# Kernel tuning notes

Measured on AMD Instinct MI355X. Metric: run time of the kernel, lower is better.

## Reference

```python
import jax, jax.numpy as jnp
import numpy as np

NQ = 10000   # num_q
N = 512      # n (seq len)
D = 512      # d (model dim)
H = 8        # attention heads
LW = 64      # local window
B = 16       # batch


def _mha(q, k, v, wi, bi, wo, bo, nh, mask=None):
    # torch nn.MultiheadAttention math (eval mode, dropout off), batch-first inputs
    Bq, S, d = q.shape
    hd = d // nh
    wq, wk, wv = jnp.split(wi, 3, axis=0)
    bq, bk, bv = jnp.split(bi, 3)

    def proj(x, w, b):
        y = x @ w.T + b
        return y.reshape(x.shape[0], x.shape[1], nh, hd).transpose(0, 2, 1, 3)  # [B,h,S,hd]

    Q = proj(q, wq, bq)
    K = proj(k, wk, bk)
    V = proj(v, wv, bv)
    s = jnp.einsum('bhqe,bhke->bhqk', Q, K) / jnp.sqrt(jnp.asarray(hd, q.dtype))
    if mask is not None:
        s = jnp.where(mask[None, None], -jnp.inf, s)
    w = jax.nn.softmax(s, axis=-1)
    o = jnp.einsum('bhqk,bhke->bhqe', w, V).transpose(0, 2, 1, 3).reshape(Bq, S, d)
    return o @ wo.T + bo, w.mean(axis=1)  # avg over heads like torch default


def _ln(x, g, b):
    m = x.mean(-1, keepdims=True)
    v = ((x - m) ** 2).mean(-1, keepdims=True)
    return (x - m) / jnp.sqrt(v + 1e-5) * g + b


def setup_inputs() -> dict:
    key = jax.random.key(0)
    ks = iter(jax.random.split(key, 40))
    f = lambda *sh: jax.random.normal(next(ks), sh, jnp.float32) * 0.02
    inp = {
        'q': jax.random.randint(next(ks), (B, N), 0, NQ, jnp.int32),
        'r': jax.random.randint(next(ks), (B, N), 0, 2, jnp.int32),
        'qry': jax.random.randint(next(ks), (B, N), 0, NQ, jnp.int32),
        'M_emb': f(2 * NQ, D),
        'E_emb': f(NQ, D),
        'P': f(N, D),
    }
    for nm in ['base', 'local', 'glob', 'cross']:
        inp[nm + '_in_w'] = f(3 * D, D)
        inp[nm + '_in_b'] = jnp.zeros((3 * D,), jnp.float32)
        inp[nm + '_out_w'] = f(D, D)
        inp[nm + '_out_b'] = jnp.zeros((D,), jnp.float32)
    inp['ln1_g'] = jnp.ones((D,), jnp.float32)
    inp['ln1_b'] = jnp.zeros((D,), jnp.float32)
    inp['w1'] = f(D, D)
    inp['b1'] = jnp.zeros((D,), jnp.float32)
    inp['w2'] = f(D, D)
    inp['b2'] = jnp.zeros((D,), jnp.float32)
    inp['ln2_g'] = jnp.ones((D,), jnp.float32)
    inp['ln2_b'] = jnp.zeros((D,), jnp.float32)
    inp['pred_w'] = f(1, D)
    inp['pred_b'] = jnp.zeros((1,), jnp.float32)
    return inp


def reference(q, r, qry, M_emb, E_emb, P,
              base_in_w, base_in_b, base_out_w, base_out_b,
              local_in_w, local_in_b, local_out_w, local_out_b,
              glob_in_w, glob_in_b, glob_out_w, glob_out_b,
              cross_in_w, cross_in_b, cross_out_w, cross_out_b,
              ln1_g, ln1_b, w1, b1, w2, b2, ln2_g, ln2_b, pred_w, pred_b):
    x = q + NQ * r
    M = M_emb[x] + P[None]          # [B,N,D], positional added as in torch code
    E = E_emb[qry]                  # [B,N,D]
    cm = jnp.triu(jnp.ones((N, N), bool), 1)

    S_base, attn_w = _mha(E, M, M, base_in_w, base_in_b, base_out_w, base_out_b, H, cm)
    S_base = _ln(S_base + M + E, ln1_g, ln1_b)

    lm = jnp.triu(jnp.ones((LW, LW), bool), 1)
    s_loc_in = S_base[:, -LW:, :]
    S_loc, _ = _mha(s_loc_in, s_loc_in, s_loc_in, local_in_w, local_in_b, local_out_w, local_out_b, H, lm)
    S_local = jnp.concatenate([jnp.zeros((S_base.shape[0], N - LW, D), S_base.dtype), S_loc], axis=1)

    S_global, _ = _mha(S_base, S_base, S_base, glob_in_w, glob_in_b, glob_out_w, glob_out_b, H, cm)
    S_cross, _ = _mha(S_base, S_local, S_local, cross_in_w, cross_in_b, cross_out_w, cross_out_b, H, None)

    S = S_base + S_local + S_global + S_cross
    F = jax.nn.relu(S @ w1.T + b1) @ w2.T + b2
    F = _ln(F + S, ln2_g, ln2_b)
    p = jax.nn.sigmoid(F @ pred_w.T + pred_b)[..., 0]   # [B,N]
    return p, attn_w
```

## Files before the change

kernel.cpp:

```cpp
#include <hip/hip_runtime.h>
#include <hip/hip_bf16.h>

#define D_MODEL 512
#define NHEAD 8
#define NSEQ 512
#define BATCH 16
#define LWIN 64
#define S2C 0.18033688f
#define L2E 1.44269504f

typedef short s16x8 __attribute__((ext_vector_type(8)));
typedef float f32x4 __attribute__((ext_vector_type(4)));

__device__ inline unsigned short f2bf(float f) {
    unsigned int u = __float_as_uint(f);
    u = (u + 0x7fffu + ((u >> 16) & 1u)) >> 16;
    return (unsigned short)u;
}
__device__ inline int sw4(int r) { return (r + (r >> 2)) & 3; }

#define GLD16(g, l) __builtin_amdgcn_global_load_lds( \
    (const __attribute__((address_space(1))) void*)(g), \
    (__attribute__((address_space(3))) void*)(l), 16, 0, 0)

struct WP { const float* p[10]; };
__global__ __launch_bounds__(256) void wconv_kernel(WP wp, unsigned short* __restrict__ Wb)
{
    const long e = ((long)blockIdx.x * 256 + threadIdx.x) * 4;
    const float* src; long loc;
    if (e < 3145728) { int rg = (int)(e / 786432); src = wp.p[rg]; loc = e - (long)rg * 786432; }
    else { long j = e - 3145728; int rg = (int)(j >> 18); src = wp.p[4 + rg]; loc = j - ((long)rg << 18); }
    float4 v = *(const float4*)(src + loc);
    ushort4 o; o.x = f2bf(v.x); o.y = f2bf(v.y); o.z = f2bf(v.z); o.w = f2bf(v.w);
    *(ushort4*)(Wb + e) = o;
}

__global__ __launch_bounds__(128) void embed_kernel(
    const int* __restrict__ q, const int* __restrict__ r, const int* __restrict__ qry,
    const float* __restrict__ M_emb, const float* __restrict__ E_emb,
    const float* __restrict__ P, float* __restrict__ Mf, float* __restrict__ Ef,
    unsigned short* __restrict__ Mb, unsigned short* __restrict__ Eb)
{
    const int t = blockIdx.x;
    const int n = t & (NSEQ - 1);
    const int x = q[t] + 10000 * r[t];
    const int e = qry[t];
    const int i = threadIdx.x;
    float4 a = ((const float4*)(M_emb + (long)x * D_MODEL))[i];
    float4 p4 = ((const float4*)(P + (long)n * D_MODEL))[i];
    float4 ev = ((const float4*)(E_emb + (long)e * D_MODEL))[i];
    float4 mv = make_float4(a.x + p4.x, a.y + p4.y, a.z + p4.z, a.w + p4.w);
    ((float4*)(Mf + (long)t * D_MODEL))[i] = mv;
    ((float4*)(Ef + (long)t * D_MODEL))[i] = ev;
    ushort4 mb; mb.x = f2bf(mv.x); mb.y = f2bf(mv.y); mb.z = f2bf(mv.z); mb.w = f2bf(mv.w);
    ushort4 eb; eb.x = f2bf(ev.x); eb.y = f2bf(ev.y); eb.z = f2bf(ev.z); eb.w = f2bf(ev.w);
    *(ushort4*)(Mb + (long)t * D_MODEL + i * 4) = mb;
    *(ushort4*)(Eb + (long)t * D_MODEL + i * 4) = eb;
}

__global__ __launch_bounds__(256) void zfill_kernel(unsigned short* __restrict__ p)
{
    const long i = ((long)blockIdx.x * 256 + threadIdx.x) * 8;
    *(uint4*)(p + i) = make_uint4(0u, 0u, 0u, 0u);
}

__global__ __launch_bounds__(256) void gemm_bf16(
    const unsigned short* __restrict__ A, const unsigned short* __restrict__ A2, int nsplit,
    const unsigned short* __restrict__ W, const float* __restrict__ bias,
    unsigned short* __restrict__ Cb, int ldcb, int crem,
    float* __restrict__ Cf, int ldcf,
    const float* __restrict__ r1, const float* __restrict__ r2, const float* __restrict__ tl,
    int relu, int arem)
{
    __shared__ __align__(16) unsigned short Sh[8704];
    unsigned short* As = Sh;
    unsigned short* Ws = Sh + 4096;
    float* Shf = (float*)Sh;

    const int tid = threadIdx.x, lane = tid & 63, wid = tid >> 6;
    const int m0 = blockIdx.y * 128, n0 = blockIdx.x * 128;
    const int mbase = (wid >> 1) * 64, nbase = (wid & 1) * 64;
    const int fr = lane & 15;
    const int lq = lane >> 4;
    const unsigned short* Asel = (n0 >= nsplit) ? A2 : A;

    const int rlane = lane >> 2, clane = lane & 3;
    const int lrA0 = wid * 16 + rlane, lrA1 = 64 + wid * 16 + rlane;
    int rgA0 = m0 + lrA0, rgA1 = m0 + lrA1;
    if (arem) {
        rgA0 = ((rgA0 >> 6) << 9) + (NSEQ - LWIN) + (rgA0 & 63);
        rgA1 = ((rgA1 >> 6) << 9) + (NSEQ - LWIN) + (rgA1 & 63);
    }
    const unsigned short* pA0 = Asel + (long)rgA0 * 512 + ((clane ^ sw4(lrA0)) << 3);
    const unsigned short* pA1 = Asel + (long)rgA1 * 512 + ((clane ^ sw4(lrA1)) << 3);
    const unsigned short* pW0 = W + (long)(n0 + lrA0) * 512 + ((clane ^ sw4(lrA0)) << 3);
    const unsigned short* pW1 = W + (long)(n0 + lrA1) * 512 + ((clane ^ sw4(lrA1)) << 3);
    unsigned short* lA0 = As + (wid * 16) * 32;
    unsigned short* lA1 = As + (64 + wid * 16) * 32;
    unsigned short* lW0 = Ws + (wid * 16) * 32;
    unsigned short* lW1 = Ws + (64 + wid * 16) * 32;

    f32x4 acc[4][4];
    #pragma unroll
    for (int i = 0; i < 4; ++i)
        #pragma unroll
        for (int j = 0; j < 4; ++j) acc[i][j] = (f32x4){0.f, 0.f, 0.f, 0.f};

    for (int k0 = 0; k0 < 512; k0 += 32) {
        __syncthreads();
        GLD16(pA0 + k0, lA0);
        GLD16(pA1 + k0, lA1);
        GLD16(pW0 + k0, lW0);
        GLD16(pW1 + k0, lW1);
        __syncthreads();

        s16x8 af[4], wf[4];
        #pragma unroll
        for (int t = 0; t < 4; ++t) {
            const int ra = mbase + t * 16 + fr;
            const int rw = nbase + t * 16 + fr;
            af[t] = *(const s16x8*)&As[ra * 32 + ((lq ^ sw4(ra)) << 3)];
            wf[t] = *(const s16x8*)&Ws[rw * 32 + ((lq ^ sw4(rw)) << 3)];
        }
        #pragma unroll
        for (int i = 0; i < 4; ++i)
            #pragma unroll
            for (int j = 0; j < 4; ++j)
                acc[i][j] = __builtin_amdgcn_mfma_f32_16x16x32_bf16(af[i], wf[j], acc[i][j], 0, 0, 0);
    }

    const int q4 = (lane >> 4) * 4;
    for (int qtr = 0; qtr < 4; ++qtr) {
        __syncthreads();
        if ((wid >> 1) == (qtr >> 1)) {
            const int ibase = (qtr & 1) * 2;
            #pragma unroll
            for (int j = 0; j < 4; ++j) {
                const int lcol = nbase + j * 16 + fr;
                const float bv = bias[n0 + lcol];
                #pragma unroll
                for (int i2 = 0; i2 < 2; ++i2) {
                    const int i = ibase + i2;
                    #pragma unroll
                    for (int rg = 0; rg < 4; ++rg) {
                        float v = acc[i][j][rg] + bv;
                        if (relu) v = fmaxf(v, 0.f);
                        Shf[((i * 16 + q4 + rg) & 31) * 132 + lcol] = v;
                    }
                }
            }
        }
        __syncthreads();
        #pragma unroll
        for (int it = 0; it < 4; ++it) {
            const int flat = it * 256 + tid;
            const int rowq = flat >> 5, k4 = flat & 31;
            const int grow = m0 + qtr * 32 + rowq;
            const int gcol = n0 + k4 * 4;
            float4 f = *(const float4*)&Shf[rowq * 132 + k4 * 4];
            if (r1) {
                float4 a = *(const float4*)(r1 + (long)grow * 512 + gcol);
                float4 b = *(const float4*)(r2 + (long)grow * 512 + gcol);
                f.x += a.x + b.x; f.y += a.y + b.y; f.z += a.z + b.z; f.w += a.w + b.w;
                const int n = grow & 511;
                if (n >= NSEQ - LWIN) {
                    float4 c = *(const float4*)(tl + ((long)(grow >> 9) * 64 + (n - (NSEQ - LWIN))) * 512 + gcol);
                    f.x += c.x; f.y += c.y; f.z += c.z; f.w += c.w;
                }
            }
            if (Cf) *(float4*)(Cf + (long)grow * ldcf + gcol) = f;
            if (Cb) {
                const int crow = crem ? (((grow >> 6) << 9) + (NSEQ - LWIN) + (grow & 63)) : grow;
                ushort4 u; u.x = f2bf(f.x); u.y = f2bf(f.y); u.z = f2bf(f.z); u.w = f2bf(f.w);
                *(ushort4*)(Cb + (long)crow * ldcb + gcol) = u;
            }
        }
    }
}

__global__ __launch_bounds__(256) void flash_mfma(
    const unsigned short* __restrict__ Q, const unsigned short* __restrict__ K,
    const unsigned short* __restrict__ V, unsigned short* __restrict__ O,
    float* __restrict__ stats, int Nq, int Nkv, int ldq, int ldkv, int causal)
{
    __shared__ __align__(16) unsigned short Ks[64 * 72];
    __shared__ __align__(16) unsigned short Pl[64 * 72];
    __shared__ __align__(16) unsigned int   Vt[64 * 36];

    const int tid = threadIdx.x, lane = tid & 63, w = tid >> 6;
    const int lm = lane & 15, lq = lane >> 4;
    const int h = blockIdx.y, b = blockIdx.z;
    const int nqt = Nq >> 6;
    const int qa = blockIdx.x, qb = nqt - 1 - qa;
    const bool single = (qa == qb);

    s16x8 aqA0, aqA1, aqB0, aqB1;
    {
        const unsigned short* qp = Q + ((long)b * Nq + qb * 64 + w * 16 + lm) * ldq + h * 64 + lq * 8;
        aqB0 = *(const s16x8*)qp; aqB1 = *(const s16x8*)(qp + 32);
    }
    if (!single) {
        const unsigned short* qp = Q + ((long)b * Nq + qa * 64 + w * 16 + lm) * ldq + h * 64 + lq * 8;
        aqA0 = *(const s16x8*)qp; aqA1 = *(const s16x8*)(qp + 32);
    }

    float mA = -INFINITY, lA = 0.f, mB = -INFINITY, lB = 0.f;
    f32x4 oA[4], oB[4];
    #pragma unroll
    for (int t = 0; t < 4; ++t) { oA[t] = (f32x4){0.f,0.f,0.f,0.f}; oB[t] = (f32x4){0.f,0.f,0.f,0.f}; }

    const int nkt = causal ? (qb + 1) : (Nkv >> 6);
    const int skey = tid >> 3, sd = (tid & 7) * 8;

    s16x8 kr0, kr1; uint4 vr0, vr1;
    {
        const long kb = ((long)b * Nkv) * ldkv + h * 64;
        kr0 = *(const s16x8*)(K + kb + (long)skey * ldkv + sd);
        kr1 = *(const s16x8*)(K + kb + (long)(skey + 32) * ldkv + sd);
        const unsigned short* vp = V + ((long)b * Nkv + 2 * skey) * ldkv + h * 64 + sd;
        vr0 = *(const uint4*)vp; vr1 = *(const uint4*)(vp + ldkv);
    }

    auto process = [&](s16x8 a0, s16x8 a1, float& m, float& l, f32x4* oacc, bool diag) {
        f32x4 sc[4];
        #pragma unroll
        for (int t = 0; t < 4; ++t) sc[t] = (f32x4){0.f,0.f,0.f,0.f};
        #pragma unroll
        for (int t = 0; t < 4; ++t) {
            s16x8 k0 = *(const s16x8*)&Ks[(t * 16 + lm) * 72 + lq * 8];
            s16x8 k1 = *(const s16x8*)&Ks[(t * 16 + lm) * 72 + lq * 8 + 32];
            sc[t] = __builtin_amdgcn_mfma_f32_16x16x32_bf16(k0, a0, sc[t], 0, 0, 0);
            sc[t] = __builtin_amdgcn_mfma_f32_16x16x32_bf16(k1, a1, sc[t], 0, 0, 0);
        }
        if (diag) {
            #pragma unroll
            for (int t = 0; t < 4; ++t)
                #pragma unroll
                for (int r = 0; r < 4; ++r)
                    if (t * 16 + lq * 4 + r > w * 16 + lm) sc[t][r] = -INFINITY;
        }
        float mt = sc[0][0];
        #pragma unroll
        for (int t = 0; t < 4; ++t)
            #pragma unroll
            for (int r = 0; r < 4; ++r) mt = fmaxf(mt, sc[t][r]);
        mt = fmaxf(mt, __shfl_xor(mt, 16));
        mt = fmaxf(mt, __shfl_xor(mt, 32));
        const float mn = fmaxf(m, mt);
        const float al = exp2f((m - mn) * S2C);
        float rs = 0.f;
        #pragma unroll
        for (int t = 0; t < 4; ++t)
            #pragma unroll
            for (int r = 0; r < 4; ++r) {
                float p = exp2f((sc[t][r] - mn) * S2C);
                sc[t][r] = p; rs += p;
            }
        rs += __shfl_xor(rs, 16);
        rs += __shfl_xor(rs, 32);
        m = mn; l = l * al + rs;
        #pragma unroll
        for (int t = 0; t < 4; ++t) oacc[t] *= al;
        #pragma unroll
        for (int t = 0; t < 4; ++t) {
            ushort4 u;
            u.x = f2bf(sc[t][0]); u.y = f2bf(sc[t][1]);
            u.z = f2bf(sc[t][2]); u.w = f2bf(sc[t][3]);
            *(ushort4*)&Pl[(w * 16 + lm) * 72 + t * 16 + lq * 4] = u;
        }
        #pragma unroll
        for (int ks = 0; ks < 2; ++ks) {
            s16x8 bp = *(const s16x8*)&Pl[(w * 16 + lm) * 72 + ks * 32 + lq * 8];
            #pragma unroll
            for (int t = 0; t < 4; ++t) {
                const int row = t * 16 + lm;
                const int pg = ((lq >> 1) + 2 * ks) ^ ((row >> 3) & 3);
                s16x8 av = *(const s16x8*)((const unsigned short*)Vt + row * 72 + pg * 16 + (lq & 1) * 8);
                oacc[t] = __builtin_amdgcn_mfma_f32_16x16x32_bf16(av, bp, oacc[t], 0, 0, 0);
            }
        }
    };

    for (int kt = 0; kt < nkt; ++kt) {
        __syncthreads();
        *(s16x8*)&Ks[skey * 72 + sd] = kr0;
        *(s16x8*)&Ks[(skey + 32) * 72 + sd] = kr1;
        {
            unsigned pw[8];
            pw[0] = (vr0.x & 0xffffu) | (vr1.x << 16);
            pw[1] = (vr0.x >> 16)     | (vr1.x & 0xffff0000u);
            pw[2] = (vr0.y & 0xffffu) | (vr1.y << 16);
            pw[3] = (vr0.y >> 16)     | (vr1.y & 0xffff0000u);
            pw[4] = (vr0.z & 0xffffu) | (vr1.z << 16);
            pw[5] = (vr0.z >> 16)     | (vr1.z & 0xffff0000u);
            pw[6] = (vr0.w & 0xffffu) | (vr1.w << 16);
            pw[7] = (vr0.w >> 16)     | (vr1.w & 0xffff0000u);
            #pragma unroll
            for (int j = 0; j < 8; ++j) {
                const int row = sd + j;
                const int col = (((skey >> 3) ^ ((row >> 3) & 3)) << 3) | (skey & 7);
                Vt[row * 36 + col] = pw[j];
            }
        }
        __syncthreads();
        if (kt + 1 < nkt) {
            const long kb = ((long)b * Nkv + (kt + 1) * 64) * ldkv + h * 64;
            kr0 = *(const s16x8*)(K + kb + (long)skey * ldkv + sd);
            kr1 = *(const s16x8*)(K + kb + (long)(skey + 32) * ldkv + sd);
            const unsigned short* vp = V + ((long)b * Nkv + (kt + 1) * 64 + 2 * skey) * ldkv + h * 64 + sd;
            vr0 = *(const uint4*)vp; vr1 = *(const uint4*)(vp + ldkv);
        }
        process(aqB0, aqB1, mB, lB, oB, causal && (kt == qb));
        if (!single && (!causal || kt <= qa))
            process(aqA0, aqA1, mA, lA, oA, causal && (kt == qa));
    }

    {
        const float inv = 1.0f / lB;
        const long orow = ((long)b * Nq + qb * 64 + w * 16 + lm) * D_MODEL + h * 64;
        #pragma unroll
        for (int t = 0; t < 4; ++t) {
            ushort4 u;
            u.x = f2bf(oB[t][0] * inv); u.y = f2bf(oB[t][1] * inv);
            u.z = f2bf(oB[t][2] * inv); u.w = f2bf(oB[t][3] * inv);
            *(ushort4*)(O + orow + t * 16 + lq * 4) = u;
        }
    }
    if (!single) {
        const float inv = 1.0f / lA;
        const long orow = ((long)b * Nq + qa * 64 + w * 16 + lm) * D_MODEL + h * 64;
        #pragma unroll
        for (int t = 0; t < 4; ++t) {
            ushort4 u;
            u.x = f2bf(oA[t][0] * inv); u.y = f2bf(oA[t][1] * inv);
            u.z = f2bf(oA[t][2] * inv); u.w = f2bf(oA[t][3] * inv);
            *(ushort4*)(O + orow + t * 16 + lq * 4) = u;
        }
    }
    if (stats && lq == 0) {
        long idx = (((long)b * NHEAD + h) * Nq + qb * 64 + w * 16 + lm) * 2;
        stats[idx] = mB * 0.125f; stats[idx + 1] = lB;
        if (!single) {
            idx = (((long)b * NHEAD + h) * Nq + qa * 64 + w * 16 + lm) * 2;
            stats[idx] = mA * 0.125f; stats[idx + 1] = lA;
        }
    }
}

__global__ __launch_bounds__(256) void attn_w_kernel(
    const unsigned short* __restrict__ Q, const unsigned short* __restrict__ K,
    const float* __restrict__ stats, float* __restrict__ AW, int ldq, int ldk)
{
    const int kt = blockIdx.x, qt = blockIdx.y, b = blockIdx.z;
    const int tid = threadIdx.x;
    if (kt > qt) {
        const int tx = tid & 15, ty = tid >> 4;
        #pragma unroll
        for (int i = 0; i < 4; ++i)
            *(float4*)(AW + ((long)b * NSEQ + qt * 64 + ty * 4 + i) * NSEQ + kt * 64 + tx * 4)
                = make_float4(0.f, 0.f, 0.f, 0.f);
        return;
    }
    __shared__ __align__(16) unsigned short Ks[64 * 72];
    const int lane = tid & 63, w = tid >> 6;
    const int lm = lane & 15, lq = lane >> 4;
    const int skey = tid >> 3, sd = (tid & 7) * 8;
    const long qrow = (long)b * NSEQ + qt * 64 + w * 16 + lm;

    f32x4 aw[4];
    #pragma unroll
    for (int t = 0; t < 4; ++t) aw[t] = (f32x4){0.f,0.f,0.f,0.f};

    for (int h = 0; h < NHEAD; ++h) {
        __syncthreads();
        {
            const long kb = ((long)b * NSEQ + kt * 64) * ldk + h * 64;
            *(s16x8*)&Ks[skey * 72 + sd] = *(const s16x8*)(K + kb + (long)skey * ldk + sd);
            *(s16x8*)&Ks[(skey + 32) * 72 + sd] = *(const s16x8*)(K + kb + (long)(skey + 32) * ldk + sd);
        }
        __syncthreads();
        s16x8 a0, a1;
        {
            const unsigned short* qp = Q + qrow * ldq + h * 64 + lq * 8;
            a0 = *(const s16x8*)qp; a1 = *(const s16x8*)(qp + 32);
        }
        f32x4 sc[4];
        #pragma unroll
        for (int t = 0; t < 4; ++t) sc[t] = (f32x4){0.f,0.f,0.f,0.f};
        #pragma unroll
        for (int t = 0; t < 4; ++t) {
            s16x8 k0 = *(const s16x8*)&Ks[(t * 16 + lm) * 72 + lq * 8];
            s16x8 k1 = *(const s16x8*)&Ks[(t * 16 + lm) * 72 + lq * 8 + 32];
            sc[t] = __builtin_amdgcn_mfma_f32_16x16x32_bf16(k0, a0, sc[t], 0, 0, 0);
            sc[t] = __builtin_amdgcn_mfma_f32_16x16x32_bf16(k1, a1, sc[t], 0, 0, 0);
        }
        float2 ml = *(const float2*)(stats + (((long)b * NHEAD + h) * NSEQ + qt * 64 + w * 16 + lm) * 2);
        const float mb2 = ml.x * L2E;
        const float sca = 0.125f / ml.y;
        #pragma unroll
        for (int t = 0; t < 4; ++t)
            #pragma unroll
            for (int r = 0; r < 4; ++r) {
                const bool masked = (kt == qt) && (t * 16 + lq * 4 + r > w * 16 + lm);
                if (!masked) aw[t][r] += exp2f(sc[t][r] * S2C - mb2) * sca;
            }
    }
    #pragma unroll
    for (int t = 0; t < 4; ++t)
        *(float4*)(AW + qrow * NSEQ + kt * 64 + t * 16 + lq * 4) = float4{aw[t][0], aw[t][1], aw[t][2], aw[t][3]};
}

__global__ __launch_bounds__(256) void ln_kernel(
    const float* __restrict__ X, const float* __restrict__ R1,
    const float* __restrict__ R2, const float* __restrict__ g,
    const float* __restrict__ bb, float* __restrict__ outf,
    unsigned short* __restrict__ outb,
    const float* __restrict__ pw, const float* __restrict__ pb,
    float* __restrict__ outp)
{
    const long row = blockIdx.x;
    const int tid = threadIdx.x;
    __shared__ float red[256];
    const long base = row * D_MODEL;
    float v0 = X[base + tid], v1 = X[base + tid + 256];
    if (R1) { v0 += R1[base + tid]; v1 += R1[base + tid + 256]; }
    if (R2) { v0 += R2[base + tid]; v1 += R2[base + tid + 256]; }
    red[tid] = v0 + v1; __syncthreads();
    for (int s = 128; s > 0; s >>= 1) {
        if (tid < s) red[tid] += red[tid + s];
        __syncthreads();
    }
    const float mean = red[0] * (1.f / 512.f);
    __syncthreads();
    const float d0 = v0 - mean, d1 = v1 - mean;
    red[tid] = d0 * d0 + d1 * d1; __syncthreads();
    for (int s = 128; s > 0; s >>= 1) {
        if (tid < s) red[tid] += red[tid + s];
        __syncthreads();
    }
    const float rstd = rsqrtf(red[0] * (1.f / 512.f) + 1e-5f);
    const float y0 = d0 * rstd * g[tid] + bb[tid];
    const float y1 = d1 * rstd * g[tid + 256] + bb[tid + 256];
    if (pw) {
        float s = y0 * pw[tid] + y1 * pw[tid + 256];
        __syncthreads();
        red[tid] = s; __syncthreads();
        for (int st = 128; st > 0; st >>= 1) {
            if (tid < st) red[tid] += red[tid + st];
            __syncthreads();
        }
        if (tid == 0) outp[row] = 1.f / (1.f + __expf(-(red[0] + pb[0])));
        return;
    }
    if (outf) { outf[base + tid] = y0; outf[base + tid + 256] = y1; }
    if (outb) { outb[base + tid] = f2bf(y0); outb[base + tid + 256] = f2bf(y1); }
}

extern "C" void kernel_launch(void* const* d_in, const int* in_sizes, int n_in,
                              void* d_out, int out_size, void* d_ws, size_t ws_size,
                              hipStream_t stream)
{
    const int*   q          = (const int*)d_in[0];
    const int*   r          = (const int*)d_in[1];
    const int*   qry        = (const int*)d_in[2];
    const float* M_emb      = (const float*)d_in[3];
    const float* E_emb      = (const float*)d_in[4];
    const float* P          = (const float*)d_in[5];
    const float* base_in_w  = (const float*)d_in[6];
    const float* base_in_b  = (const float*)d_in[7];
    const float* base_out_w = (const float*)d_in[8];
    const float* base_out_b = (const float*)d_in[9];
    const float* local_in_w = (const float*)d_in[10];
    const float* local_in_b = (const float*)d_in[11];
    const float* local_out_w= (const float*)d_in[12];
    const float* local_out_b= (const float*)d_in[13];
    const float* glob_in_w  = (const float*)d_in[14];
    const float* glob_in_b  = (const float*)d_in[15];
    const float* glob_out_w = (const float*)d_in[16];
    const float* glob_out_b = (const float*)d_in[17];
    const float* cross_in_w = (const float*)d_in[18];
    const float* cross_in_b = (const float*)d_in[19];
    const float* cross_out_w= (const float*)d_in[20];
    const float* cross_out_b= (const float*)d_in[21];
    const float* ln1_g      = (const float*)d_in[22];
    const float* ln1_b      = (const float*)d_in[23];
    const float* w1         = (const float*)d_in[24];
    const float* b1         = (const float*)d_in[25];
    const float* w2         = (const float*)d_in[26];
    const float* b2         = (const float*)d_in[27];
    const float* ln2_g      = (const float*)d_in[28];
    const float* ln2_b      = (const float*)d_in[29];
    const float* pred_w     = (const float*)d_in[30];
    const float* pred_b     = (const float*)d_in[31];
    float* out = (float*)d_out;

    char* p = (char*)d_ws;
    unsigned short* Wb = (unsigned short*)p; p += 4718592L * 2;
    unsigned short* B[11];
    for (int i = 0; i < 11; ++i) { B[i] = (unsigned short*)p; p += 8388608L; }
    unsigned short* Obl  = (unsigned short*)p; p += 1048576L;
    float* R[4];
    for (int i = 0; i < 4; ++i) { R[i] = (float*)p; p += 16777216L; }
    float* Tloc  = (float*)p; p += 2097152L;
    float* stats = (float*)p; p += 524288L;

    unsigned short* Mb = B[0];
    unsigned short* Eb = B[1];      unsigned short* Oc_b = B[1];
    unsigned short* QKVb = B[2];
    unsigned short* Sb_b = B[2];
    unsigned short* Ob  = B[5];
    unsigned short* Sbase_b  = B[6];
    unsigned short* Slocal_b = B[7];
    unsigned short* QKV3 = B[8];
    unsigned short* H1_b = B[8];
    float* Mf = R[0];
    float* Ef = R[1];       float* Sbuf_f   = R[1];
    float* Tb_f = R[2];     float* Sglobal_f= R[2];
    float* Sbase_f = R[3];  float* Fpre_f   = R[3];

    const long oBin = 0, oLin = 786432, oGin = 1572864, oCin = 2359296;
    const long oBout = 3145728, oLout = 3407872, oGout = 3670016, oCout = 3932160;
    const long oW1 = 4194304, oW2 = 4456448;
    const int BIG = 1 << 30;
    const unsigned short* NUS = nullptr;
    const float* NF = nullptr;

    dim3 gN512(4, 64), gN1536(12, 64);
    dim3 gL1536(12, 8), gL512(4, 8);
    dim3 fa_full(4, NHEAD, BATCH), fa_loc(1, NHEAD, BATCH);

    WP wp; wp.p[0] = base_in_w; wp.p[1] = local_in_w; wp.p[2] = glob_in_w; wp.p[3] = cross_in_w;
    wp.p[4] = base_out_w; wp.p[5] = local_out_w; wp.p[6] = glob_out_w; wp.p[7] = cross_out_w;
    wp.p[8] = w1; wp.p[9] = w2;
    wconv_kernel<<<4608, 256, 0, stream>>>(wp, Wb);
    zfill_kernel<<<2048, 256, 0, stream>>>(Slocal_b);

    embed_kernel<<<8192, 128, 0, stream>>>(q, r, qry, M_emb, E_emb, P, Mf, Ef, Mb, Eb);

    gemm_bf16<<<gN1536, 256, 0, stream>>>(Eb, Mb, 512, Wb + oBin, base_in_b,
        QKVb, 1536, 0, nullptr, 0, NF, NF, NF, 0, 0);
    flash_mfma<<<fa_full, 256, 0, stream>>>(QKVb, QKVb + 512, QKVb + 1024, Ob, stats, 512, 512, 1536, 1536, 1);
    attn_w_kernel<<<dim3(8, 8, BATCH), 256, 0, stream>>>(QKVb, QKVb + 512, stats, out + 8192, 1536, 1536);
    gemm_bf16<<<gN512, 256, 0, stream>>>(Ob, NUS, BIG, Wb + oBout, base_out_b,
        nullptr, 0, 0, Tb_f, 512, NF, NF, NF, 0, 0);
    ln_kernel<<<8192, 256, 0, stream>>>(Tb_f, Mf, Ef, ln1_g, ln1_b, Sbase_f, Sbase_b, NF, NF, nullptr);

    gemm_bf16<<<gL1536, 256, 0, stream>>>(Sbase_b, NUS, BIG, Wb + oLin, local_in_b,
        QKV3, 1536, 0, nullptr, 0, NF, NF, NF, 0, 1);
    flash_mfma<<<fa_loc, 256, 0, stream>>>(QKV3, QKV3 + 512, QKV3 + 1024, Obl, nullptr, 64, 64, 1536, 1536, 1);
    gemm_bf16<<<gL512, 256, 0, stream>>>(Obl, NUS, BIG, Wb + oLout, local_out_b,
        Slocal_b, 512, 1, Tloc, 512, NF, NF, NF, 0, 0);

    gemm_bf16<<<gN1536, 256, 0, stream>>>(Sbase_b, NUS, BIG, Wb + oGin, glob_in_b,
        QKV3, 1536, 0, nullptr, 0, NF, NF, NF, 0, 0);
    flash_mfma<<<fa_full, 256, 0, stream>>>(QKV3, QKV3 + 512, QKV3 + 1024, Ob, nullptr, 512, 512, 1536, 1536, 1);
    gemm_bf16<<<gN512, 256, 0, stream>>>(Ob, NUS, BIG, Wb + oGout, glob_out_b,
        nullptr, 0, 0, Sglobal_f, 512, NF, NF, NF, 0, 0);

    gemm_bf16<<<gN1536, 256, 0, stream>>>(Sbase_b, Slocal_b, 512, Wb + oCin, cross_in_b,
        QKVb, 1536, 0, nullptr, 0, NF, NF, NF, 0, 0);
    flash_mfma<<<fa_full, 256, 0, stream>>>(QKVb, QKVb + 512, QKVb + 1024, Oc_b, nullptr, 512, 512, 1536, 1536, 0);
    gemm_bf16<<<gN512, 256, 0, stream>>>(Oc_b, NUS, BIG, Wb + oCout, cross_out_b,
        Sb_b, 512, 0, Sbuf_f, 512, Sbase_f, Sglobal_f, Tloc, 0, 0);

    gemm_bf16<<<gN512, 256, 0, stream>>>(Sb_b, NUS, BIG, Wb + oW1, b1,
        H1_b, 512, 0, nullptr, 0, NF, NF, NF, 1, 0);
    gemm_bf16<<<gN512, 256, 0, stream>>>(H1_b, NUS, BIG, Wb + oW2, b2,
        nullptr, 0, 0, Fpre_f, 512, NF, NF, NF, 0, 0);
    ln_kernel<<<8192, 256, 0, stream>>>(Fpre_f, Sbuf_f, nullptr, ln2_g, ln2_b,
        nullptr, nullptr, pred_w, pred_b, out);
}
```

Baseline: 526.7 us.

## Load GEMM MFMA operands directly from global memory instead of LDS staging

The bf16 GEMM main loop no longer stages A and W tiles into shared memory through global_load_lds with barriers. Each lane now loads its MFMA fragments straight from global memory, and the loop is unrolled by two. This removes two barriers per k-step and the LDS round trip. In exchange, operands are no longer shared between waves: each A and W row is fetched by two waves, which doubles global and L2 traffic and gives less coalescing, with no explicit prefetch to hide latency.

```diff
diff --git a/kernel.cpp b/kernel.cpp
--- a/kernel.cpp
+++ b/kernel.cpp
@@ -17,11 +17,6 @@
     u = (u + 0x7fffu + ((u >> 16) & 1u)) >> 16;
     return (unsigned short)u;
 }
-__device__ inline int sw4(int r) { return (r + (r >> 2)) & 3; }
-
-#define GLD16(g, l) __builtin_amdgcn_global_load_lds( \
-    (const __attribute__((address_space(1))) void*)(g), \
-    (__attribute__((address_space(3))) void*)(l), 16, 0, 0)
 
 struct WP { const float* p[10]; };
 __global__ __launch_bounds__(256) void wconv_kernel(WP wp, unsigned short* __restrict__ Wb)
@@ -72,33 +67,24 @@
     const float* __restrict__ r1, const float* __restrict__ r2, const float* __restrict__ tl,
     int relu, int arem)
 {
-    __shared__ __align__(16) unsigned short Sh[8704];
-    unsigned short* As = Sh;
-    unsigned short* Ws = Sh + 4096;
-    float* Shf = (float*)Sh;
+    __shared__ __align__(16) float Shf[32 * 132];
 
     const int tid = threadIdx.x, lane = tid & 63, wid = tid >> 6;
     const int m0 = blockIdx.y * 128, n0 = blockIdx.x * 128;
     const int mbase = (wid >> 1) * 64, nbase = (wid & 1) * 64;
-    const int fr = lane & 15;
+    const int lm = lane & 15;
     const int lq = lane >> 4;
     const unsigned short* Asel = (n0 >= nsplit) ? A2 : A;
 
-    const int rlane = lane >> 2, clane = lane & 3;
-    const int lrA0 = wid * 16 + rlane, lrA1 = 64 + wid * 16 + rlane;
-    int rgA0 = m0 + lrA0, rgA1 = m0 + lrA1;
-    if (arem) {
-        rgA0 = ((rgA0 >> 6) << 9) + (NSEQ - LWIN) + (rgA0 & 63);
-        rgA1 = ((rgA1 >> 6) << 9) + (NSEQ - LWIN) + (rgA1 & 63);
-    }
-    const unsigned short* pA0 = Asel + (long)rgA0 * 512 + ((clane ^ sw4(lrA0)) << 3);
-    const unsigned short* pA1 = Asel + (long)rgA1 * 512 + ((clane ^ sw4(lrA1)) << 3);
-    const unsigned short* pW0 = W + (long)(n0 + lrA0) * 512 + ((clane ^ sw4(lrA0)) << 3);
-    const unsigned short* pW1 = W + (long)(n0 + lrA1) * 512 + ((clane ^ sw4(lrA1)) << 3);
-    unsigned short* lA0 = As + (wid * 16) * 32;
-    unsigned short* lA1 = As + (64 + wid * 16) * 32;
-    unsigned short* lW0 = Ws + (wid * 16) * 32;
-    unsigned short* lW1 = Ws + (64 + wid * 16) * 32;
+    const unsigned short* pa[4];
+    const unsigned short* pw[4];
+    #pragma unroll
+    for (int t = 0; t < 4; ++t) {
+        int ra = m0 + mbase + t * 16 + lm;
+        if (arem) ra = ((ra >> 6) << 9) + (NSEQ - LWIN) + (ra & 63);
+        pa[t] = Asel + (long)ra * 512 + lq * 8;
+        pw[t] = W + (long)(n0 + nbase + t * 16 + lm) * 512 + lq * 8;
+    }
 
     f32x4 acc[4][4];
     #pragma unroll
@@ -106,21 +92,13 @@
         #pragma unroll
         for (int j = 0; j < 4; ++j) acc[i][j] = (f32x4){0.f, 0.f, 0.f, 0.f};
 
+    #pragma unroll 2
     for (int k0 = 0; k0 < 512; k0 += 32) {
-        __syncthreads();
-        GLD16(pA0 + k0, lA0);
-        GLD16(pA1 + k0, lA1);
-        GLD16(pW0 + k0, lW0);
-        GLD16(pW1 + k0, lW1);
-        __syncthreads();
-
         s16x8 af[4], wf[4];
         #pragma unroll
         for (int t = 0; t < 4; ++t) {
-            const int ra = mbase + t * 16 + fr;
-            const int rw = nbase + t * 16 + fr;
-            af[t] = *(const s16x8*)&As[ra * 32 + ((lq ^ sw4(ra)) << 3)];
-            wf[t] = *(const s16x8*)&Ws[rw * 32 + ((lq ^ sw4(rw)) << 3)];
+            af[t] = *(const s16x8*)(pa[t] + k0);
+            wf[t] = *(const s16x8*)(pw[t] + k0);
         }
         #pragma unroll
         for (int i = 0; i < 4; ++i)
@@ -129,6 +107,7 @@
                 acc[i][j] = __builtin_amdgcn_mfma_f32_16x16x32_bf16(af[i], wf[j], acc[i][j], 0, 0, 0);
     }
 
+    const int fr = lane & 15;
     const int q4 = (lane >> 4) * 4;
     for (int qtr = 0; qtr < 4; ++qtr) {
         __syncthreads();
```

Result: slower. 670.7 us (+27.3%).
